# Performance work log

Hardware: AMD Instinct MI355X
Metric: run time of the kernel (lower is better)

The kernel has to match this reference:

```python
import jax, jax.numpy as jnp
import numpy as np

L, H, NH, HD, FF = 4, 1024, 16, 64, 4096
EPS = 1e-5
NEG = jnp.finfo(jnp.float32).min


def _ln(x, g, b):
    m = x.mean(-1, keepdims=True)
    v = ((x - m) ** 2).mean(-1, keepdims=True)
    return (x - m) * jax.lax.rsqrt(v + EPS) * g + b


def _rotate_half(x):
    # interleaved: out[...,0::2] = -x[...,1::2]; out[...,1::2] = x[...,0::2]
    x1 = x[..., ::2]
    x2 = x[..., 1::2]
    return jnp.stack((-x2, x1), axis=-1).reshape(x.shape)


def _rope_cos_sin(position_ids):
    # position_ids: [B,S] int -> cos/sin [B,S,1,HD] (freqs repeated interleaved)
    inv_freq = 1.0 / (10000.0 ** (jnp.arange(0, HD, 2, dtype=jnp.float32) / HD))
    freqs = position_ids.astype(jnp.float32)[..., None] * inv_freq  # [B,S,HD/2]
    emb = jnp.repeat(freqs, 2, axis=-1)  # [B,S,HD]
    return jnp.cos(emb)[:, :, None, :], jnp.sin(emb)[:, :, None, :]


def _apply_rope(x, cos, sin):
    return x * cos + _rotate_half(x) * sin


def setup_inputs() -> dict:
    key = jax.random.key(0)
    ks = jax.random.split(key, 8)
    s = 0.02
    inp = {
        "inputs_embeds": jax.random.normal(ks[0], (4, 1024, H), jnp.float32),
        "attention_mask": jnp.ones((4, 1024), dtype=bool),
        "Wqkv": jax.random.normal(ks[1], (L, H, 3 * H), jnp.float32) * s,
        "bqkv": jnp.zeros((L, 3 * H), jnp.float32),
        "Wo": jax.random.normal(ks[2], (L, H, H), jnp.float32) * s,
        "bo": jnp.zeros((L, H), jnp.float32),
        "ln1_g": jnp.ones((L, H), jnp.float32),
        "ln1_b": jnp.zeros((L, H), jnp.float32),
        "ln2_g": jnp.ones((L, H), jnp.float32),
        "ln2_b": jnp.zeros((L, H), jnp.float32),
        "Wfc": jax.random.normal(ks[3], (L, H, FF), jnp.float32) * s,
        "bfc": jnp.zeros((L, FF), jnp.float32),
        "Wproj": jax.random.normal(ks[4], (L, FF, H), jnp.float32) * s,
        "bproj": jnp.zeros((L, H), jnp.float32),
        "lnf_g": jnp.ones((H,), jnp.float32),
        "lnf_b": jnp.zeros((H,), jnp.float32),
    }
    return inp


def reference(inputs_embeds, attention_mask, Wqkv, bqkv, Wo, bo, ln1_g, ln1_b,
              ln2_g, ln2_b, Wfc, bfc, Wproj, bproj, lnf_g, lnf_b):
    B, S, _ = inputs_embeds.shape
    mask = attention_mask  # bool [B,S]
    maskf = mask.astype(inputs_embeds.dtype)[:, :, None]  # [B,S,1]

    # position ids from mask (cumsum - 1, clamped to 0 on pad)
    pid = jnp.cumsum(mask.astype(jnp.int32), axis=-1) - 1
    pid = jnp.where(mask, pid, 0)
    cos, sin = _rope_cos_sin(pid)

    # causal + padding mask: [B,1,S,S]
    qpos = jnp.arange(S)
    causal = (qpos[None, :] <= qpos[:, None])[None, None]  # [1,1,S,S]
    amask = causal & mask[:, None, None, :]

    scale = 1.0 / (HD ** 0.5)
    h = inputs_embeds * maskf  # drop() is identity in eval

    for l in range(L):
        hs = _ln(h, ln1_g[l], ln1_b[l])
        qkv = hs @ Wqkv[l] + bqkv[l]
        q, k, v = jnp.split(qkv, 3, axis=-1)
        q = _apply_rope(q.reshape(B, S, NH, HD), cos, sin)
        k = _apply_rope(k.reshape(B, S, NH, HD), cos, sin)
        v = v.reshape(B, S, NH, HD)
        scores = jnp.einsum("bqhd,bkhd->bhqk", q, k) * scale
        scores = jnp.where(amask, scores, NEG)
        probs = jax.nn.softmax(scores, axis=-1)
        attn = jnp.einsum("bhqk,bkhd->bqhd", probs, v).reshape(B, S, H)
        attn = attn @ Wo[l] + bo[l]
        h = h + attn
        m = _ln(h, ln2_g[l], ln2_b[l])
        m = jax.nn.gelu(m @ Wfc[l] + bfc[l], approximate=True) @ Wproj[l] + bproj[l]
        h = (h + m) * maskf

    h = _ln(h, lnf_g, lnf_b) * maskf
    return h
```

## Files before the change

### kernel.cpp

```cpp
#include <hip/hip_runtime.h>
#include <math.h>


typedef unsigned short u16;
typedef unsigned int u32;
typedef __attribute__((ext_vector_type(8))) short short8;
typedef __attribute__((ext_vector_type(4))) float f32x4;
typedef __attribute__((ext_vector_type(4))) u16 u16x4;

#define NEGV (-3.402823466e38f)

__device__ __forceinline__ u16 f2bf(float f) {
  union { float f; u32 u; } v; v.f = f;
  u32 r = v.u + 0x7FFFu + ((v.u >> 16) & 1u);
  return (u16)(r >> 16);
}

__device__ __forceinline__ float gelu_tanh(float x) {
  float z = 0.7978845608028654f * (x + 0.044715f * x * x * x);
  z = fmaxf(fminf(z, 30.f), -30.f);
  float t = __expf(2.f * z);
  return 0.5f * x * (1.f + (t - 1.f) / (t + 1.f));
}

__device__ __forceinline__ void gld_lds16(const u16* g, u16* l) {
  __builtin_amdgcn_global_load_lds((const __attribute__((address_space(1))) u32*)g,
                                   (__attribute__((address_space(3))) u32*)l, 16, 0, 0);
}

__global__ __launch_bounds__(1024) void mask_pid_kernel(const void* __restrict__ maskp,
                                                        float* __restrict__ maskf,
                                                        int* __restrict__ pid) {
  int b = blockIdx.x, s = threadIdx.x;
  const u32* wp = (const u32*)maskp;
  bool int_mode = ((wp[0] & 0xFFFFFF00u) == 0u);
  int mv;
  if (int_mode) mv = (((const int*)maskp)[b * 1024 + s] != 0) ? 1 : 0;
  else          mv = (((const unsigned char*)maskp)[b * 1024 + s] != 0) ? 1 : 0;
  __shared__ int sc[1024];
  sc[s] = mv;
  __syncthreads();
  for (int off = 1; off < 1024; off <<= 1) {
    int add = (s >= off) ? sc[s - off] : 0;
    __syncthreads();
    sc[s] += add;
    __syncthreads();
  }
  pid[b * 1024 + s] = mv ? (sc[s] - 1) : 0;
  maskf[b * 1024 + s] = (float)mv;
}

__global__ __launch_bounds__(256) void embed_kernel(const float* __restrict__ e,
                                                    const float* __restrict__ maskf,
                                                    float* __restrict__ h) {
  int idx = blockIdx.x * 256 + threadIdx.x;
  size_t o = (size_t)idx * 4;
  int row = (int)(o >> 10);
  float mf = maskf[row];
  float4 v = *(const float4*)(e + o);
  float4 r; r.x = v.x * mf; r.y = v.y * mf; r.z = v.z * mf; r.w = v.w * mf;
  *(float4*)(h + o) = r;
}

__global__ __launch_bounds__(256) void transpose_bf16(const float* __restrict__ in,
                                                      u16* __restrict__ out,
                                                      int K, int N) {
  __shared__ float t[32][33];
  int tx = threadIdx.x, ty = threadIdx.y;
  int n0 = blockIdx.x * 32, k0 = blockIdx.y * 32;
#pragma unroll
  for (int j = 0; j < 4; ++j) {
    int k = ty + j * 8;
    t[k][tx] = in[(size_t)(k0 + k) * N + n0 + tx];
  }
  __syncthreads();
#pragma unroll
  for (int j = 0; j < 4; ++j) {
    int n = ty + j * 8;
    out[(size_t)(n0 + n) * K + k0 + tx] = f2bf(t[tx][n]);
  }
}

template <int MODE>
__global__ __launch_bounds__(256) void ln_kernel(const float* __restrict__ x,
                                                 const float* __restrict__ g,
                                                 const float* __restrict__ bb,
                                                 u16* __restrict__ yb,
                                                 float* __restrict__ yf,
                                                 const float* __restrict__ maskf) {
  int row = blockIdx.x, tid = threadIdx.x;
  const float* xr = x + (size_t)row * 1024;
  float4 v = *(const float4*)(xr + tid * 4);
  float s = v.x + v.y + v.z + v.w;
  float q = v.x * v.x + v.y * v.y + v.z * v.z + v.w * v.w;
#pragma unroll
  for (int off = 32; off >= 1; off >>= 1) {
    s += __shfl_xor(s, off);
    q += __shfl_xor(q, off);
  }
  __shared__ float ps[4], pq[4];
  int w = tid >> 6, lane = tid & 63;
  if (lane == 0) { ps[w] = s; pq[w] = q; }
  __syncthreads();
  float S = ps[0] + ps[1] + ps[2] + ps[3];
  float Q = pq[0] + pq[1] + pq[2] + pq[3];
  float mean = S * (1.f / 1024.f);
  float var = fmaxf(Q * (1.f / 1024.f) - mean * mean, 0.f);
  float rstd = rsqrtf(var + 1e-5f);
  int c = tid * 4;
  float4 gv = *(const float4*)(g + c);
  float4 bv = *(const float4*)(bb + c);
  float y0 = (v.x - mean) * rstd * gv.x + bv.x;
  float y1 = (v.y - mean) * rstd * gv.y + bv.y;
  float y2 = (v.z - mean) * rstd * gv.z + bv.z;
  float y3 = (v.w - mean) * rstd * gv.w + bv.w;
  if (MODE == 0) {
    u16x4 o; o.x = f2bf(y0); o.y = f2bf(y1); o.z = f2bf(y2); o.w = f2bf(y3);
    *(u16x4*)(yb + (size_t)row * 1024 + c) = o;
  } else {
    float mf = maskf[row];
    float4 o; o.x = y0 * mf; o.y = y1 * mf; o.z = y2 * mf; o.w = y3 * mf;
    *(float4*)(yf + (size_t)row * 1024 + c) = o;
  }
}

template <int EPI>
__global__ __launch_bounds__(256) void gemm128(const u16* __restrict__ A,
                                               const u16* __restrict__ Bt,
                                               const float* __restrict__ bias,
                                               float* __restrict__ Of,
                                               u16* __restrict__ Ob,
                                               const float* __restrict__ maskf,
                                               int M, int N, int K) {
  __shared__ __align__(16) u16 As[128 * 32];
  __shared__ __align__(16) u16 Bs[128 * 32];
  const int tid = threadIdx.x;
  const int lane = tid & 63, w = tid >> 6;
  const int wm = w >> 1, wn = w & 1;
  const int m0 = blockIdx.y * 128, n0 = blockIdx.x * 128;
  const int ln = lane & 15, kg = lane >> 4;

  f32x4 acc[4][4] = {};

  const int r0 = tid >> 2, g0 = (tid & 3) * 8;
  const u16* Ap0 = A + (size_t)(m0 + r0) * K + g0;
  const u16* Ap1 = A + (size_t)(m0 + 64 + r0) * K + g0;
  const u16* Bp0 = Bt + (size_t)(n0 + r0) * K + g0;
  const u16* Bp1 = Bt + (size_t)(n0 + 64 + r0) * K + g0;
  u16* AsD0 = As + tid * 8;
  u16* AsD1 = As + (tid + 256) * 8;
  u16* BsD0 = Bs + tid * 8;
  u16* BsD1 = Bs + (tid + 256) * 8;

  for (int k0 = 0; k0 < K; k0 += 32) {
    __syncthreads();
    gld_lds16(Ap0 + k0, AsD0);
    gld_lds16(Ap1 + k0, AsD1);
    gld_lds16(Bp0 + k0, BsD0);
    gld_lds16(Bp1 + k0, BsD1);
    __syncthreads();

    short8 af[4], bfr[4];
#pragma unroll
    for (int mt = 0; mt < 4; ++mt)
      af[mt] = *(const short8*)(As + (wm * 64 + mt * 16 + ln) * 32 + kg * 8);
#pragma unroll
    for (int nt = 0; nt < 4; ++nt)
      bfr[nt] = *(const short8*)(Bs + (wn * 64 + nt * 16 + ln) * 32 + kg * 8);
#pragma unroll
    for (int mt = 0; mt < 4; ++mt)
#pragma unroll
      for (int nt = 0; nt < 4; ++nt)
        acc[mt][nt] = __builtin_amdgcn_mfma_f32_16x16x32_bf16(af[mt], bfr[nt], acc[mt][nt], 0, 0, 0);
  }

#pragma unroll
  for (int mt = 0; mt < 4; ++mt) {
#pragma unroll
    for (int nt = 0; nt < 4; ++nt) {
      int col = n0 + wn * 64 + nt * 16 + ln;
      float bvv = bias[col];
#pragma unroll
      for (int rr = 0; rr < 4; ++rr) {
        int row = m0 + wm * 64 + mt * 16 + kg * 4 + rr;
        size_t idx = (size_t)row * N + col;
        float v = acc[mt][nt][rr] + bvv;
        if (EPI == 0) {
          Of[idx] = v;
        } else if (EPI == 1) {
          Of[idx] += v;
        } else if (EPI == 2) {
          Ob[idx] = f2bf(gelu_tanh(v));
        } else {
          Of[idx] = (Of[idx] + v) * maskf[row];
        }
      }
    }
  }
}

__global__ __launch_bounds__(256) void rope_kernel(const float* __restrict__ qkv,
                                                   const int* __restrict__ pid,
                                                   u16* __restrict__ qh,
                                                   u16* __restrict__ kh,
                                                   u16* __restrict__ vh) {
  int idx = blockIdx.x * 256 + threadIdx.x;
  int i = idx & 31;
  int hh = (idx >> 5) & 15;
  int row = idx >> 9;
  int b = row >> 10, s = row & 1023;
  float p = (float)pid[row];
  float inv = __expf(-(float)(2 * i) * (9.210340371976184f / 64.f));
  float th = p * inv;
  float c = cosf(th), sn = sinf(th);
  size_t base = (size_t)row * 3072 + hh * 64 + 2 * i;
  float q0 = qkv[base], q1 = qkv[base + 1];
  float k0 = qkv[base + 1024], k1 = qkv[base + 1025];
  float v0 = qkv[base + 2048], v1 = qkv[base + 2049];
  float qr0 = (q0 * c - q1 * sn) * 0.125f;
  float qr1 = (q1 * c + q0 * sn) * 0.125f;
  float kr0 = k0 * c - k1 * sn;
  float kr1 = k1 * c + k0 * sn;
  size_t hbase = ((size_t)(b * 16 + hh) * 1024 + s) * 64 + 2 * i;
  *(u32*)(qh + hbase) = (u32)f2bf(qr0) | ((u32)f2bf(qr1) << 16);
  *(u32*)(kh + hbase) = (u32)f2bf(kr0) | ((u32)f2bf(kr1) << 16);
  *(u32*)(vh + hbase) = (u32)f2bf(v0) | ((u32)f2bf(v1) << 16);
}

__global__ __launch_bounds__(256) void attn_mfma(const u16* __restrict__ qh,
                                                 const u16* __restrict__ kh,
                                                 const u16* __restrict__ vh,
                                                 const float* __restrict__ maskf,
                                                 u16* __restrict__ ctx) {
  const int b = blockIdx.z, h = blockIdx.y, qt = blockIdx.x;
  const int tid = threadIdx.x, lane = tid & 63, w = tid >> 6;
  const int ln = lane & 15, kg = lane >> 4;
  const int q0 = qt * 64;
  const size_t hb = (size_t)(b * 16 + h) * 1024 * 64;

  __shared__ __align__(16) u16 Ks[64][72];
  __shared__ __align__(16) u16 VsT[64][72];
  __shared__ __align__(16) u16 Ps[64][72];
  __shared__ float Ms[64];

  const int qrow = q0 + w * 16 + ln;
  short8 qa0 = *(const short8*)(qh + hb + (size_t)qrow * 64 + kg * 8);
  short8 qa1 = *(const short8*)(qh + hb + (size_t)qrow * 64 + 32 + kg * 8);

  f32x4 Oc[4] = {};
  float m_i[4], l_i[4];
#pragma unroll
  for (int r = 0; r < 4; ++r) { m_i[r] = NEGV; l_i[r] = 0.f; }

  const int ntiles = qt + 1;
  for (int t = 0; t < ntiles; ++t) {
    __syncthreads();
    {
      int row = tid >> 2, c8 = (tid & 3) * 8;
      const u16* kp2 = kh + hb + (size_t)(t * 64 + row) * 64;
      *(uint4*)(&Ks[row][c8]) = *(const uint4*)(kp2 + c8);
      *(uint4*)(&Ks[row][c8 + 32]) = *(const uint4*)(kp2 + c8 + 32);
    }
    {
      int kp = tid >> 3, dg = tid & 7;
      const u16* vp0 = vh + hb + (size_t)(t * 64 + 2 * kp) * 64 + dg * 8;
      uint4 r0 = *(const uint4*)vp0;
      uint4 r1 = *(const uint4*)(vp0 + 64);
      u32 a0[4] = {r0.x, r0.y, r0.z, r0.w};
      u32 a1[4] = {r1.x, r1.y, r1.z, r1.w};
#pragma unroll
      for (int j = 0; j < 8; ++j) {
        u32 lo = (a0[j >> 1] >> (16 * (j & 1))) & 0xffffu;
        u32 hi = (a1[j >> 1] >> (16 * (j & 1))) & 0xffffu;
        *(u32*)(&VsT[dg * 8 + j][2 * kp]) = lo | (hi << 16);
      }
    }
    if (tid < 64) Ms[tid] = maskf[b * 1024 + t * 64 + tid];
    __syncthreads();

    f32x4 Sc[4];
#pragma unroll
    for (int c = 0; c < 4; ++c) {
      short8 kb0 = *(const short8*)(&Ks[c * 16 + ln][kg * 8]);
      short8 kb1 = *(const short8*)(&Ks[c * 16 + ln][32 + kg * 8]);
      f32x4 z = {};
      z = __builtin_amdgcn_mfma_f32_16x16x32_bf16(qa0, kb0, z, 0, 0, 0);
      Sc[c] = __builtin_amdgcn_mfma_f32_16x16x32_bf16(qa1, kb1, z, 0, 0, 0);
    }
    float mk[4];
#pragma unroll
    for (int c = 0; c < 4; ++c) mk[c] = Ms[c * 16 + ln];

#pragma unroll
    for (int r = 0; r < 4; ++r) {
      int qg = q0 + w * 16 + kg * 4 + r;
      float vmax = NEGV;
#pragma unroll
      for (int c = 0; c < 4; ++c) {
        int key = t * 64 + c * 16 + ln;
        bool valid = (key <= qg) && (mk[c] != 0.f);
        float sv = valid ? Sc[c][r] : NEGV;
        Sc[c][r] = sv;
        vmax = fmaxf(vmax, sv);
      }
#pragma unroll
      for (int off = 1; off <= 8; off <<= 1) vmax = fmaxf(vmax, __shfl_xor(vmax, off));
      float mnew = fmaxf(m_i[r], vmax);
      float alpha = __expf(m_i[r] - mnew);
      m_i[r] = mnew;
      float ls = 0.f;
#pragma unroll
      for (int c = 0; c < 4; ++c) {
        float p = __expf(Sc[c][r] - mnew);
        Sc[c][r] = p;
        ls += p;
      }
#pragma unroll
      for (int off = 1; off <= 8; off <<= 1) ls += __shfl_xor(ls, off);
      l_i[r] = l_i[r] * alpha + ls;
#pragma unroll
      for (int c = 0; c < 4; ++c) Oc[c][r] *= alpha;
#pragma unroll
      for (int c = 0; c < 4; ++c) Ps[w * 16 + kg * 4 + r][c * 16 + ln] = f2bf(Sc[c][r]);
    }
    __syncthreads();

    short8 pa0 = *(const short8*)(&Ps[w * 16 + ln][kg * 8]);
    short8 pa1 = *(const short8*)(&Ps[w * 16 + ln][32 + kg * 8]);
#pragma unroll
    for (int c = 0; c < 4; ++c) {
      short8 vb0 = *(const short8*)(&VsT[c * 16 + ln][kg * 8]);
      short8 vb1 = *(const short8*)(&VsT[c * 16 + ln][32 + kg * 8]);
      Oc[c] = __builtin_amdgcn_mfma_f32_16x16x32_bf16(pa0, vb0, Oc[c], 0, 0, 0);
      Oc[c] = __builtin_amdgcn_mfma_f32_16x16x32_bf16(pa1, vb1, Oc[c], 0, 0, 0);
    }
  }

#pragma unroll
  for (int r = 0; r < 4; ++r) {
    float rl = 1.f / l_i[r];
    int row = q0 + w * 16 + kg * 4 + r;
#pragma unroll
    for (int c = 0; c < 4; ++c) {
      ctx[(size_t)(b * 1024 + row) * 1024 + h * 64 + c * 16 + ln] = f2bf(Oc[c][r] * rl);
    }
  }
}

extern "C" void kernel_launch(void* const* d_in, const int* in_sizes, int n_in,
                              void* d_out, int out_size, void* d_ws, size_t ws_size,
                              hipStream_t stream) {
  const float* embeds = (const float*)d_in[0];
  const void* amask   = d_in[1];
  const float* Wqkv = (const float*)d_in[2];
  const float* bqkv = (const float*)d_in[3];
  const float* Wo   = (const float*)d_in[4];
  const float* bo   = (const float*)d_in[5];
  const float* ln1g = (const float*)d_in[6];
  const float* ln1b = (const float*)d_in[7];
  const float* ln2g = (const float*)d_in[8];
  const float* ln2b = (const float*)d_in[9];
  const float* Wfc  = (const float*)d_in[10];
  const float* bfc  = (const float*)d_in[11];
  const float* Wpj  = (const float*)d_in[12];
  const float* bpj  = (const float*)d_in[13];
  const float* lnfg = (const float*)d_in[14];
  const float* lnfb = (const float*)d_in[15];
  float* out = (float*)d_out;

  char* ws = (char*)d_ws;
  float* h     = (float*)(ws);
  float* qkv   = (float*)(ws + (size_t)(16u << 20));
  u16*   xb    = (u16*)(ws + (size_t)(64u << 20));
  u16*   ffb   = (u16*)(ws + (size_t)(72u << 20));
  u16*   qhp   = (u16*)(ws + (size_t)(72u << 20));
  u16*   khp   = (u16*)(ws + (size_t)(80u << 20));
  u16*   vhp   = (u16*)(ws + (size_t)(88u << 20));
  u16*   wqT   = (u16*)(ws + (size_t)(104u << 20));
  u16*   woT   = (u16*)(ws + (size_t)(110u << 20));
  u16*   wfT   = (u16*)(ws + (size_t)(112u << 20));
  u16*   wpT   = (u16*)(ws + (size_t)(120u << 20));
  float* maskf = (float*)(ws + (size_t)(128u << 20));
  int*   pid   = (int*)(ws + (size_t)(128u << 20) + (16u << 10));

  mask_pid_kernel<<<4, 1024, 0, stream>>>(amask, maskf, pid);
  embed_kernel<<<4096, 256, 0, stream>>>(embeds, maskf, h);

  for (int l = 0; l < 4; ++l) {
    transpose_bf16<<<dim3(96, 32), dim3(32, 8), 0, stream>>>(Wqkv + (size_t)l * 1024 * 3072, wqT, 1024, 3072);
    transpose_bf16<<<dim3(32, 32), dim3(32, 8), 0, stream>>>(Wo + (size_t)l * 1024 * 1024, woT, 1024, 1024);
    transpose_bf16<<<dim3(128, 32), dim3(32, 8), 0, stream>>>(Wfc + (size_t)l * 1024 * 4096, wfT, 1024, 4096);
    transpose_bf16<<<dim3(32, 128), dim3(32, 8), 0, stream>>>(Wpj + (size_t)l * 4096 * 1024, wpT, 4096, 1024);

    ln_kernel<0><<<4096, 256, 0, stream>>>(h, ln1g + l * 1024, ln1b + l * 1024, xb, nullptr, nullptr);
    gemm128<0><<<dim3(24, 32), 256, 0, stream>>>(xb, wqT, bqkv + l * 3072, qkv, nullptr, nullptr, 4096, 3072, 1024);
    rope_kernel<<<8192, 256, 0, stream>>>(qkv, pid, qhp, khp, vhp);
    attn_mfma<<<dim3(16, 16, 4), 256, 0, stream>>>(qhp, khp, vhp, maskf, xb);
    gemm128<1><<<dim3(8, 32), 256, 0, stream>>>(xb, woT, bo + l * 1024, h, nullptr, nullptr, 4096, 1024, 1024);
    ln_kernel<0><<<4096, 256, 0, stream>>>(h, ln2g + l * 1024, ln2b + l * 1024, xb, nullptr, nullptr);
    gemm128<2><<<dim3(32, 32), 256, 0, stream>>>(xb, wfT, bfc + l * 4096, nullptr, ffb, nullptr, 4096, 4096, 1024);
    gemm128<3><<<dim3(8, 32), 256, 0, stream>>>(ffb, wpT, bpj + l * 1024, h, nullptr, maskf, 4096, 1024, 4096);
  }
  ln_kernel<1><<<4096, 256, 0, stream>>>(h, lnfg, lnfb, nullptr, out, maskf);
}
```

Measured before the change: 1.598 ms.

## Double-buffer GEMM LDS tiles, XOR-swizzle LDS, remap blocks for XCD locality

The GEMM now double-buffers its A/B tiles in LDS. The next k-slice is issued with direct global-to-LDS loads before the MFMAs on the current one, which drops one barrier per iteration and overlaps load latency with compute. It also XOR-swizzles the k-group offset, applied the same way on store and read, to cut LDS bank conflicts on the short8 fragment reads. The launch becomes a 1D grid with a custom bid-to-(m,n) mapping that groups M tiles, likely to improve L2 and XCD locality of B-tile reuse. LDS use doubles to 32KB per block, which may lower occupancy.

```diff
diff --git a/kernel.cpp b/kernel.cpp
--- a/kernel.cpp
+++ b/kernel.cpp
@@ -132,59 +132,67 @@
                                                u16* __restrict__ Ob,
                                                const float* __restrict__ maskf,
                                                int M, int N, int K) {
-  __shared__ __align__(16) u16 As[128 * 32];
-  __shared__ __align__(16) u16 Bs[128 * 32];
+  __shared__ __align__(16) u16 As[2][128 * 32];
+  __shared__ __align__(16) u16 Bs[2][128 * 32];
   const int tid = threadIdx.x;
   const int lane = tid & 63, w = tid >> 6;
   const int wm = w >> 1, wn = w & 1;
-  const int m0 = blockIdx.y * 128, n0 = blockIdx.x * 128;
+  const int bid = blockIdx.x;
+  const int m0 = (((bid & 7) << 2) + ((bid >> 3) & 3)) << 7;
+  const int n0 = (bid >> 5) << 7;
   const int ln = lane & 15, kg = lane >> 4;
+  const int kxor = (kg ^ ((ln >> 1) & 3)) * 8;
 
   f32x4 acc[4][4] = {};
 
-  const int r0 = tid >> 2, g0 = (tid & 3) * 8;
-  const u16* Ap0 = A + (size_t)(m0 + r0) * K + g0;
-  const u16* Ap1 = A + (size_t)(m0 + 64 + r0) * K + g0;
-  const u16* Bp0 = Bt + (size_t)(n0 + r0) * K + g0;
-  const u16* Bp1 = Bt + (size_t)(n0 + 64 + r0) * K + g0;
-  u16* AsD0 = As + tid * 8;
-  u16* AsD1 = As + (tid + 256) * 8;
-  u16* BsD0 = Bs + tid * 8;
-  u16* BsD1 = Bs + (tid + 256) * 8;
-
-  for (int k0 = 0; k0 < K; k0 += 32) {
-    __syncthreads();
-    gld_lds16(Ap0 + k0, AsD0);
-    gld_lds16(Ap1 + k0, AsD1);
-    gld_lds16(Bp0 + k0, BsD0);
-    gld_lds16(Bp1 + k0, BsD1);
-    __syncthreads();
-
+  const int r0 = tid >> 2;
+  const int gsw = ((tid & 3) ^ ((tid >> 3) & 3)) * 8;
+  const u16* Ap0 = A + (size_t)(m0 + r0) * K + gsw;
+  const u16* Ap1 = A + (size_t)(m0 + 64 + r0) * K + gsw;
+  const u16* Bp0 = Bt + (size_t)(n0 + r0) * K + gsw;
+  const u16* Bp1 = Bt + (size_t)(n0 + 64 + r0) * K + gsw;
+
+  const int niter = K >> 5;
+  gld_lds16(Ap0, &As[0][tid * 8]);
+  gld_lds16(Ap1, &As[0][(tid + 256) * 8]);
+  gld_lds16(Bp0, &Bs[0][tid * 8]);
+  gld_lds16(Bp1, &Bs[0][(tid + 256) * 8]);
+
+  for (int it = 0; it < niter; ++it) {
+    __syncthreads();
+    const int cur = it & 1, nxt = cur ^ 1;
+    if (it + 1 < niter) {
+      const int k0 = (it + 1) << 5;
+      gld_lds16(Ap0 + k0, &As[nxt][tid * 8]);
+      gld_lds16(Ap1 + k0, &As[nxt][(tid + 256) * 8]);
+      gld_lds16(Bp0 + k0, &Bs[nxt][tid * 8]);
+      gld_lds16(Bp1 + k0, &Bs[nxt][(tid + 256) * 8]);
+    }
     short8 af[4], bfr[4];
 #pragma unroll
-    for (int mt = 0; mt < 4; ++mt)
-      af[mt] = *(const short8*)(As + (wm * 64 + mt * 16 + ln) * 32 + kg * 8);
-#pragma unroll
-    for (int nt = 0; nt < 4; ++nt)
-      bfr[nt] = *(const short8*)(Bs + (wn * 64 + nt * 16 + ln) * 32 + kg * 8);
-#pragma unroll
-    for (int mt = 0; mt < 4; ++mt)
-#pragma unroll
-      for (int nt = 0; nt < 4; ++nt)
-        acc[mt][nt] = __builtin_amdgcn_mfma_f32_16x16x32_bf16(af[mt], bfr[nt], acc[mt][nt], 0, 0, 0);
-  }
-
-#pragma unroll
-  for (int mt = 0; mt < 4; ++mt) {
-#pragma unroll
-    for (int nt = 0; nt < 4; ++nt) {
-      int col = n0 + wn * 64 + nt * 16 + ln;
+    for (int i = 0; i < 4; ++i)
+      af[i] = *(const short8*)(&As[cur][(wm * 64 + i * 16 + ln) * 32 + kxor]);
+#pragma unroll
+    for (int i = 0; i < 4; ++i)
+      bfr[i] = *(const short8*)(&Bs[cur][(wn * 64 + i * 16 + ln) * 32 + kxor]);
+#pragma unroll
+    for (int i = 0; i < 4; ++i)
+#pragma unroll
+      for (int j = 0; j < 4; ++j)
+        acc[i][j] = __builtin_amdgcn_mfma_f32_16x16x32_bf16(af[i], bfr[j], acc[i][j], 0, 0, 0);
+  }
+
+#pragma unroll
+  for (int i = 0; i < 4; ++i) {
+#pragma unroll
+    for (int j = 0; j < 4; ++j) {
+      int col = n0 + wn * 64 + j * 16 + ln;
       float bvv = bias[col];
 #pragma unroll
       for (int rr = 0; rr < 4; ++rr) {
-        int row = m0 + wm * 64 + mt * 16 + kg * 4 + rr;
+        int row = m0 + wm * 64 + i * 16 + kg * 4 + rr;
         size_t idx = (size_t)row * N + col;
-        float v = acc[mt][nt][rr] + bvv;
+        float v = acc[i][j][rr] + bvv;
         if (EPI == 0) {
           Of[idx] = v;
         } else if (EPI == 1) {
@@ -393,13 +401,13 @@
     transpose_bf16<<<dim3(32, 128), dim3(32, 8), 0, stream>>>(Wpj + (size_t)l * 4096 * 1024, wpT, 4096, 1024);
 
     ln_kernel<0><<<4096, 256, 0, stream>>>(h, ln1g + l * 1024, ln1b + l * 1024, xb, nullptr, nullptr);
-    gemm128<0><<<dim3(24, 32), 256, 0, stream>>>(xb, wqT, bqkv + l * 3072, qkv, nullptr, nullptr, 4096, 3072, 1024);
+    gemm128<0><<<dim3(24 * 32), 256, 0, stream>>>(xb, wqT, bqkv + l * 3072, qkv, nullptr, nullptr, 4096, 3072, 1024);
     rope_kernel<<<8192, 256, 0, stream>>>(qkv, pid, qhp, khp, vhp);
     attn_mfma<<<dim3(16, 16, 4), 256, 0, stream>>>(qhp, khp, vhp, maskf, xb);
-    gemm128<1><<<dim3(8, 32), 256, 0, stream>>>(xb, woT, bo + l * 1024, h, nullptr, nullptr, 4096, 1024, 1024);
+    gemm128<1><<<dim3(8 * 32), 256, 0, stream>>>(xb, woT, bo + l * 1024, h, nullptr, nullptr, 4096, 1024, 1024);
     ln_kernel<0><<<4096, 256, 0, stream>>>(h, ln2g + l * 1024, ln2b + l * 1024, xb, nullptr, nullptr);
-    gemm128<2><<<dim3(32, 32), 256, 0, stream>>>(xb, wfT, bfc + l * 4096, nullptr, ffb, nullptr, 4096, 4096, 1024);
-    gemm128<3><<<dim3(8, 32), 256, 0, stream>>>(ffb, wpT, bpj + l * 1024, h, nullptr, maskf, 4096, 1024, 4096);
+    gemm128<2><<<dim3(32 * 32), 256, 0, stream>>>(xb, wfT, bfc + l * 4096, nullptr, ffb, nullptr, 4096, 4096, 1024);
+    gemm128<3><<<dim3(8 * 32), 256, 0, stream>>>(ffb, wpT, bpj + l * 1024, h, nullptr, maskf, 4096, 1024, 4096);
   }
   ln_kernel<1><<<4096, 256, 0, stream>>>(h, lnfg, lnfb, nullptr, out, maskf);
 }
```

Measured after the change: 1.489 ms. 6.9% less time.
